# Kernel optimization log

Hardware: AMD Instinct MI355X
Metric: run time of the kernel (lower is better)

Reference implementation:

```python
import jax, jax.numpy as jnp
import numpy as np

D_IN = 1024
D_OUT = 1024
NUM_HEADS = 16
D_HEAD = D_OUT // NUM_HEADS


def setup_inputs() -> dict:
    key = jax.random.key(0)
    ks = jax.random.split(key, 6)
    s = 0.02
    return {
        "x": jax.random.normal(ks[0], (2, 2048, D_IN), dtype=jnp.float32),
        "W_q": jax.random.normal(ks[1], (D_IN, D_OUT), dtype=jnp.float32) * s,
        "W_k": jax.random.normal(ks[2], (D_IN, D_OUT), dtype=jnp.float32) * s,
        "W_v": jax.random.normal(ks[3], (D_IN, D_OUT), dtype=jnp.float32) * s,
        "W_o": jax.random.normal(ks[4], (D_OUT, D_OUT), dtype=jnp.float32) * s,
        "b_o": jax.random.normal(ks[5], (D_OUT,), dtype=jnp.float32) * s,
    }


def reference(x, W_q, W_k, W_v, W_o, b_o):
    B, T, _ = x.shape
    # qkv projections (no bias), split heads -> [B, H, T, d_head]
    def split_heads(t):
        return t.reshape(B, T, NUM_HEADS, D_HEAD).transpose(0, 2, 1, 3)
    q = split_heads(x @ W_q)
    k = split_heads(x @ W_k)
    v = split_heads(x @ W_v)
    # full causal scores [B, H, T, T]
    scores = jnp.einsum("bhqd,bhkd->bhqk", q, k)
    causal = jnp.triu(jnp.ones((T, T), dtype=bool), k=1)
    scores = jnp.where(causal, -jnp.inf, scores)
    attn = jax.nn.softmax(scores / np.sqrt(D_HEAD).astype(np.float32), axis=-1)
    # dropout rate is 0.0 -> identity
    ctx = jnp.einsum("bhqk,bhkd->bhqd", attn, v)
    ctx = ctx.transpose(0, 2, 1, 3).reshape(B, T, D_OUT)
    return ctx @ W_o + b_o
```

## Files before the change

kernel.cpp:

```cpp
#include <hip/hip_runtime.h>
#include <hip/hip_bf16.h>
#include <cstdint>

#define SEQ_T 2048
#define DMODEL 1024
#define NHEAD 16
#define DHEAD 64

typedef __attribute__((ext_vector_type(8))) __bf16 bf16x8;
typedef __attribute__((ext_vector_type(4))) float floatx4;

static __device__ __forceinline__ uint16_t f2bf(float f) {
    union { float f; uint32_t u; } v; v.f = f;
    uint32_t r = v.u + 0x7FFFu + ((v.u >> 16) & 1u);
    return (uint16_t)(r >> 16);
}

__global__ void mha_cvt(const float* __restrict__ x, uint16_t* __restrict__ xb,
                        const float* __restrict__ W0, const float* __restrict__ W1,
                        const float* __restrict__ W2, const float* __restrict__ W3,
                        uint16_t* __restrict__ T0, uint16_t* __restrict__ T1,
                        uint16_t* __restrict__ T2, uint16_t* __restrict__ T3) {
    if (blockIdx.z == 4) {
        int base = (blockIdx.y * 16 + blockIdx.x) * 256 + threadIdx.x;
#pragma unroll
        for (int i = 0; i < 16; ++i) {
            int idx = base + i * 65536;
            float4 f = ((const float4*)x)[idx];
            union { uint16_t u[4]; uint64_t v; } o;
            o.u[0] = f2bf(f.x); o.u[1] = f2bf(f.y); o.u[2] = f2bf(f.z); o.u[3] = f2bf(f.w);
            ((uint64_t*)xb)[idx] = o.v;
        }
        return;
    }
    const float* W; uint16_t* Tt; float sc;
    switch (blockIdx.z) {
        case 0: W = W0; Tt = T0; sc = 0.125f * 1.44269504089f; break;
        case 1: W = W1; Tt = T1; sc = 1.f; break;
        case 2: W = W2; Tt = T2; sc = 1.f; break;
        default: W = W3; Tt = T3; sc = 1.f; break;
    }
    __shared__ float tile[64][65];
    const int c  = threadIdx.x & 63;
    const int r0 = threadIdx.x >> 6;
    const int R0 = blockIdx.y * 64, C0 = blockIdx.x * 64;
#pragma unroll
    for (int rr = 0; rr < 16; ++rr) {
        int r = r0 + rr * 4;
        tile[r][c] = W[(size_t)(R0 + r) * DMODEL + C0 + c];
    }
    __syncthreads();
#pragma unroll
    for (int rr = 0; rr < 16; ++rr) {
        int r = r0 + rr * 4;
        Tt[(size_t)(C0 + r) * DMODEL + R0 + c] = f2bf(tile[c][r] * sc);
    }
}

template<int MODE>
__device__ __forceinline__ void gemm_bk64_body(
    const uint16_t* __restrict__ A, const uint16_t* __restrict__ Bt,
    uint16_t* __restrict__ outB) {
    const int K = DMODEL, N = DMODEL;
    extern __shared__ char smem[];
    uint16_t* As = (uint16_t*)smem;
    uint16_t* Bs = (uint16_t*)(smem + 8192);
    const int tid  = threadIdx.x;
    const int wave = tid >> 6;
    const int lane = tid & 63;
    const int m0 = blockIdx.y * 64;
    const int n0 = blockIdx.x * 128;
    const int lr   = lane & 15;
    const int quad = lane >> 4;

    floatx4 acc[4][2];
#pragma unroll
    for (int i = 0; i < 4; ++i)
#pragma unroll
        for (int j = 0; j < 2; ++j) acc[i][j] = (floatx4)0.0f;

    for (int k0 = 0; k0 < K; k0 += 64) {
#pragma unroll
        for (int i = 0; i < 2; ++i) {
            int c = i * 256 + tid;
            int r = c >> 3, s = (c & 7) ^ (r & 7);
            const uint16_t* g = A + (size_t)(m0 + r) * K + k0 + s * 8;
            __builtin_amdgcn_global_load_lds((const __attribute__((address_space(1))) void*)g,
                                             (__attribute__((address_space(3))) void*)(As + (size_t)c * 8), 16, 0, 0);
        }
#pragma unroll
        for (int i = 0; i < 4; ++i) {
            int c = i * 256 + tid;
            int r = c >> 3, s = (c & 7) ^ (r & 7);
            const uint16_t* g = Bt + (size_t)(n0 + r) * K + k0 + s * 8;
            __builtin_amdgcn_global_load_lds((const __attribute__((address_space(1))) void*)g,
                                             (__attribute__((address_space(3))) void*)(Bs + (size_t)c * 8), 16, 0, 0);
        }
        __syncthreads();
#pragma unroll
        for (int ks = 0; ks < 2; ++ks) {
            bf16x8 af[4], bfr[2];
#pragma unroll
            for (int mi = 0; mi < 4; ++mi) {
                int row = mi * 16 + lr;
                af[mi] = *(const bf16x8*)&As[row * 64 + (((ks * 4 + quad) ^ (row & 7)) << 3)];
            }
#pragma unroll
            for (int ni = 0; ni < 2; ++ni) {
                int row = wave * 32 + ni * 16 + lr;
                bfr[ni] = *(const bf16x8*)&Bs[row * 64 + (((ks * 4 + quad) ^ (row & 7)) << 3)];
            }
#pragma unroll
            for (int mi = 0; mi < 4; ++mi)
#pragma unroll
                for (int ni = 0; ni < 2; ++ni)
                    acc[mi][ni] = __builtin_amdgcn_mfma_f32_16x16x32_bf16(af[mi], bfr[ni], acc[mi][ni], 0, 0, 0);
        }
        __syncthreads();
    }
    if constexpr (MODE == 1) {
        uint16_t* Ct = (uint16_t*)smem;
        const int bb = m0 >> 11, t0 = m0 & 2047;
#pragma unroll
        for (int mi = 0; mi < 4; ++mi)
#pragma unroll
            for (int ni = 0; ni < 2; ++ni) {
                int cl = wave * 32 + ni * 16 + lr;
                int tl = mi * 16 + quad * 4;
                int tls = tl ^ ((cl & 3) << 4);
                union { uint16_t u[4]; uint64_t v8; } pk;
#pragma unroll
                for (int r = 0; r < 4; ++r) pk.u[r] = f2bf(acc[mi][ni][r]);
                *(uint64_t*)&Ct[cl * 72 + tls] = pk.v8;
            }
        __syncthreads();
#pragma unroll
        for (int k = 0; k < 4; ++k) {
            int c = k * 256 + tid;
            int cl = c >> 3, off = (c & 7) * 8;
            int offs = off ^ ((cl & 3) << 4);
            uint4 v = *(const uint4*)&Ct[cl * 72 + offs];
            *(uint4*)&outB[((size_t)(bb * 1024 + n0 + cl)) * 2048 + t0 + off] = v;
        }
    } else {
#pragma unroll
        for (int mi = 0; mi < 4; ++mi)
#pragma unroll
            for (int ni = 0; ni < 2; ++ni) {
                int col = n0 + wave * 32 + ni * 16 + lr;
#pragma unroll
                for (int r = 0; r < 4; ++r) {
                    int row = m0 + mi * 16 + quad * 4 + r;
                    outB[(size_t)row * N + col] = f2bf(acc[mi][ni][r]);
                }
            }
    }
}

__global__ __launch_bounds__(256) void mha_gemm_qkv(
    const uint16_t* __restrict__ A,
    const uint16_t* __restrict__ Wq, const uint16_t* __restrict__ Wk, const uint16_t* __restrict__ Wv,
    uint16_t* __restrict__ Q, uint16_t* __restrict__ K, uint16_t* __restrict__ Vt) {
    switch (blockIdx.z) {
        case 0:  gemm_bk64_body<0>(A, Wq, Q);  break;
        case 1:  gemm_bk64_body<0>(A, Wk, K);  break;
        default: gemm_bk64_body<1>(A, Wv, Vt); break;
    }
}

__global__ __launch_bounds__(512) void mha_gemm_out(
    const uint16_t* __restrict__ A, const uint16_t* __restrict__ Wot,
    float* __restrict__ out, const float* __restrict__ bias) {
    const int K = DMODEL, N = DMODEL;
    extern __shared__ char smem[];
    uint16_t* As = (uint16_t*)smem;
    uint16_t* Bs = (uint16_t*)(smem + 8192);
    const int tid  = threadIdx.x;
    const int wave = tid >> 6;
    const int lane = tid & 63;
    const int m0 = blockIdx.y * 64;
    const int n0 = blockIdx.x * 128;
    const int lr   = lane & 15;
    const int quad = lane >> 4;
    const int wm = wave >> 2, wn = wave & 3;

    floatx4 acc[2][2];
#pragma unroll
    for (int i = 0; i < 2; ++i)
#pragma unroll
        for (int j = 0; j < 2; ++j) acc[i][j] = (floatx4)0.0f;

    for (int k0 = 0; k0 < K; k0 += 64) {
        {
            int c = tid;
            int r = c >> 3, s = (c & 7) ^ (r & 7);
            const uint16_t* g = A + (size_t)(m0 + r) * K + k0 + s * 8;
            __builtin_amdgcn_global_load_lds((const __attribute__((address_space(1))) void*)g,
                                             (__attribute__((address_space(3))) void*)(As + (size_t)c * 8), 16, 0, 0);
        }
#pragma unroll
        for (int i = 0; i < 2; ++i) {
            int c = i * 512 + tid;
            int r = c >> 3, s = (c & 7) ^ (r & 7);
            const uint16_t* g = Wot + (size_t)(n0 + r) * K + k0 + s * 8;
            __builtin_amdgcn_global_load_lds((const __attribute__((address_space(1))) void*)g,
                                             (__attribute__((address_space(3))) void*)(Bs + (size_t)c * 8), 16, 0, 0);
        }
        __syncthreads();
#pragma unroll
        for (int ks = 0; ks < 2; ++ks) {
            bf16x8 af[2], bfr[2];
#pragma unroll
            for (int mi = 0; mi < 2; ++mi) {
                int row = wm * 32 + mi * 16 + lr;
                af[mi] = *(const bf16x8*)&As[row * 64 + (((ks * 4 + quad) ^ (row & 7)) << 3)];
            }
#pragma unroll
            for (int ni = 0; ni < 2; ++ni) {
                int row = wn * 32 + ni * 16 + lr;
                bfr[ni] = *(const bf16x8*)&Bs[row * 64 + (((ks * 4 + quad) ^ (row & 7)) << 3)];
            }
#pragma unroll
            for (int mi = 0; mi < 2; ++mi)
#pragma unroll
                for (int ni = 0; ni < 2; ++ni)
                    acc[mi][ni] = __builtin_amdgcn_mfma_f32_16x16x32_bf16(af[mi], bfr[ni], acc[mi][ni], 0, 0, 0);
        }
        __syncthreads();
    }
#pragma unroll
    for (int mi = 0; mi < 2; ++mi)
#pragma unroll
        for (int ni = 0; ni < 2; ++ni) {
            int col = n0 + wn * 32 + ni * 16 + lr;
            float bv = bias[col];
#pragma unroll
            for (int r = 0; r < 4; ++r) {
                int row = m0 + wm * 32 + mi * 16 + quad * 4 + r;
                out[(size_t)row * N + col] = acc[mi][ni][r] + bv;
            }
        }
}

__global__ __launch_bounds__(256) void mha_attn_mfma(
    const uint16_t* __restrict__ Q, const uint16_t* __restrict__ K,
    const uint16_t* __restrict__ Vt, uint16_t* __restrict__ ctx) {
    __shared__ alignas(16) uint16_t Ks[3][64 * 64];
    __shared__ alignas(16) uint16_t Vs[3][64 * 64];
    __shared__ alignas(16) uint16_t Pb[64 * 64];

    const int tid  = threadIdx.x;
    const int wave = tid >> 6;
    const int lane = tid & 63;
    const int lr   = lane & 15;
    const int quad = lane >> 4;
    const int h  = blockIdx.x;
    const int p  = blockIdx.y;
    const int b  = blockIdx.z;
    const int jH = 31 - p, jL = p;
    const int TH = jH + 1;
    const int TL = jL + 1;
    const int Ttot = TH + TL;

    const uint16_t* kbase[2];
    const uint16_t* vbase[2];
#pragma unroll
    for (int i = 0; i < 2; ++i) {
        int c = i * 256 + tid;
        int row = c >> 3, cs = c & 7;
        int csk = cs ^ (row & 7);
        kbase[i] = K  + ((size_t)(b * SEQ_T) + row) * DMODEL + h * DHEAD + csk * 8;
        vbase[i] = Vt + ((size_t)(b * 1024 + h * DHEAD + row)) * 2048 + csk * 8;
    }

    int wrow = jH * 64 + wave * 16;
    bf16x8 qf0, qf1;
    {
        const size_t qb = ((size_t)(b * SEQ_T) + wrow + lr) * DMODEL + h * DHEAD;
        qf0 = *(const bf16x8*)(Q + qb + quad * 8);
        qf1 = *(const bf16x8*)(Q + qb + 32 + quad * 8);
    }
    bf16x8 ones;
#pragma unroll
    for (int i = 0; i < 8; ++i) ones[i] = (__bf16)1.0f;

    floatx4 o[4];
#pragma unroll
    for (int nt = 0; nt < 4; ++nt) o[nt] = (floatx4)0.0f;
    floatx4 lacc = (floatx4)0.0f;

    auto kvof = [&](int t) { return ((t < TH) ? t : (t - TH)) * 64; };
    auto stage = [&](int kv0, int buf) {
#pragma unroll
        for (int i = 0; i < 2; ++i) {
            const uint16_t* gk = kbase[i] + (size_t)kv0 * DMODEL;
            const uint16_t* gv = vbase[i] + kv0;
            uint16_t* lk = &Ks[buf][(i * 256 + wave * 64) * 8];
            uint16_t* lv = &Vs[buf][(i * 256 + wave * 64) * 8];
            __builtin_amdgcn_global_load_lds((const __attribute__((address_space(1))) void*)gk,
                                             (__attribute__((address_space(3))) void*)lk, 16, 0, 0);
            __builtin_amdgcn_global_load_lds((const __attribute__((address_space(1))) void*)gv,
                                             (__attribute__((address_space(3))) void*)lv, 16, 0, 0);
        }
    };
    auto epilogue = [&]() {
        float linv[4];
#pragma unroll
        for (int r = 0; r < 4; ++r) linv[r] = 1.f / lacc[r];
#pragma unroll
        for (int nt = 0; nt < 4; ++nt)
#pragma unroll
            for (int r = 0; r < 4; ++r) {
                size_t addr = ((size_t)(b * SEQ_T) + wrow + quad * 4 + r) * DMODEL + h * DHEAD + nt * 16 + lr;
                ctx[addr] = f2bf(o[nt][r] * linv[r]);
            }
    };

    stage(kvof(0), 0);
    stage(kvof(1), 1);
    __builtin_amdgcn_s_waitcnt(0x0F74);
    __builtin_amdgcn_s_barrier();

    for (int t = 0; t < Ttot; ++t) {
        if (t + 2 < Ttot) stage(kvof(t + 2), (t + 2) % 3);
        const int cur = t % 3;
        const int kv0 = kvof(t);

        floatx4 s[4];
#pragma unroll
        for (int nt = 0; nt < 4; ++nt) {
            s[nt] = (floatx4)0.0f;
            int krow = nt * 16 + lr;
#pragma unroll
            for (int ks = 0; ks < 2; ++ks) {
                bf16x8 kf = *(const bf16x8*)&Ks[cur][krow * 64 + (((ks * 4 + quad) ^ (lr & 7)) * 8)];
                s[nt] = __builtin_amdgcn_mfma_f32_16x16x32_bf16(ks ? qf1 : qf0, kf, s[nt], 0, 0, 0);
            }
        }
        if (kv0 + 63 > wrow) {
#pragma unroll
            for (int nt = 0; nt < 4; ++nt) {
                int kcol = kv0 + nt * 16 + lr;
#pragma unroll
                for (int r = 0; r < 4; ++r) {
                    int qrow = wrow + quad * 4 + r;
                    if (kcol > qrow) s[nt][r] = -3e38f;
                }
            }
        }
#pragma unroll
        for (int nt = 0; nt < 4; ++nt)
#pragma unroll
            for (int r = 0; r < 4; ++r) {
                float pe = __builtin_amdgcn_exp2f(s[nt][r]);
                int row = wave * 16 + quad * 4 + r;
                int cc  = (nt * 2 + (lr >> 3)) ^ (row & 7);
                Pb[row * 64 + cc * 8 + (lr & 7)] = (uint16_t)(__float_as_uint(pe) >> 16);
            }
#pragma unroll
        for (int ks = 0; ks < 2; ++ks) {
            int prow = wave * 16 + lr;
            bf16x8 pfr = *(const bf16x8*)&Pb[prow * 64 + (((ks * 4 + quad) ^ (prow & 7)) * 8)];
            lacc = __builtin_amdgcn_mfma_f32_16x16x32_bf16(pfr, ones, lacc, 0, 0, 0);
#pragma unroll
            for (int nt = 0; nt < 4; ++nt) {
                int vrow = nt * 16 + lr;
                bf16x8 vf = *(const bf16x8*)&Vs[cur][vrow * 64 + (((ks * 4 + quad) ^ (lr & 7)) * 8)];
                o[nt] = __builtin_amdgcn_mfma_f32_16x16x32_bf16(pfr, vf, o[nt], 0, 0, 0);
            }
        }
        if (t == TH - 1) {
            epilogue();
            wrow = jL * 64 + wave * 16;
            const size_t qb = ((size_t)(b * SEQ_T) + wrow + lr) * DMODEL + h * DHEAD;
            qf0 = *(const bf16x8*)(Q + qb + quad * 8);
            qf1 = *(const bf16x8*)(Q + qb + 32 + quad * 8);
#pragma unroll
            for (int nt = 0; nt < 4; ++nt) o[nt] = (floatx4)0.0f;
            lacc = (floatx4)0.0f;
        }
        if (t + 2 < Ttot) {
            __builtin_amdgcn_s_waitcnt(0x0F74);
            __builtin_amdgcn_s_barrier();
        } else if (t + 1 < Ttot) {
            __builtin_amdgcn_s_waitcnt(0x0F70);
            __builtin_amdgcn_s_barrier();
        }
    }
    epilogue();
}

extern "C" void kernel_launch(void* const* d_in, const int* in_sizes, int n_in,
                              void* d_out, int out_size, void* d_ws, size_t ws_size,
                              hipStream_t stream) {
    const float* x  = (const float*)d_in[0];
    const float* Wq = (const float*)d_in[1];
    const float* Wk = (const float*)d_in[2];
    const float* Wv = (const float*)d_in[3];
    const float* Wo = (const float*)d_in[4];
    const float* bo = (const float*)d_in[5];
    float* out = (float*)d_out;

    char* ws = (char*)d_ws;
    const size_t SZ_X = (size_t)4096 * DMODEL * 2;
    const size_t SZ_W = (size_t)DMODEL * DMODEL * 2;
    size_t off = 0;
    uint16_t* xb  = (uint16_t*)(ws + off); off += SZ_X;
    uint16_t* wqt = (uint16_t*)(ws + off); off += SZ_W;
    uint16_t* wkt = (uint16_t*)(ws + off); off += SZ_W;
    uint16_t* wvt = (uint16_t*)(ws + off); off += SZ_W;
    uint16_t* wot = (uint16_t*)(ws + off); off += SZ_W;
    uint16_t* Qb  = (uint16_t*)(ws + off); off += SZ_X;
    uint16_t* Kb  = (uint16_t*)(ws + off); off += SZ_X;
    uint16_t* Vtb = (uint16_t*)(ws + off); off += SZ_X;
    uint16_t* Cb  = (uint16_t*)(ws + off); off += SZ_X;
    (void)ws_size; (void)in_sizes; (void)n_in; (void)out_size;

    mha_cvt<<<dim3(16, 16, 5), 256, 0, stream>>>(x, xb, Wq, Wk, Wv, Wo, wqt, wkt, wvt, wot);
    mha_gemm_qkv<<<dim3(8, 64, 3), 256, 24576, stream>>>(xb, wqt, wkt, wvt, Qb, Kb, Vtb);
    mha_attn_mfma<<<dim3(NHEAD, 16, 2), 256, 0, stream>>>(Qb, Kb, Vtb, Cb);
    mha_gemm_out<<<dim3(8, 64), 512, 24576, stream>>>(Cb, wot, out, bo);
}
```

Measured before the change: 177.5 us.

## Split attention KV tiles across two wave groups with 128-wide tiles and LDS combine

The attention kernel moves to 512 threads. Two groups of four waves each handle half of a 128-key tile, so each block needs fewer sequential iterations (17 instead of up to 33) and keeps double buffering in place of triple buffering. Partial outputs and row sums from the second group are combined through LDS before the store. In exchange there are extra barriers and LDS traffic at the combine, larger LDS tiles that may lower occupancy, and masking now covers whole 128 tiles, which can waste work on the diagonal.

```diff
diff --git a/kernel.cpp b/kernel.cpp
--- a/kernel.cpp
+++ b/kernel.cpp
@@ -242,38 +242,38 @@
         }
 }
 
-__global__ __launch_bounds__(256) void mha_attn_mfma(
+__global__ __launch_bounds__(512, 4) void mha_attn_mfma(
     const uint16_t* __restrict__ Q, const uint16_t* __restrict__ K,
     const uint16_t* __restrict__ Vt, uint16_t* __restrict__ ctx) {
-    __shared__ alignas(16) uint16_t Ks[3][64 * 64];
-    __shared__ alignas(16) uint16_t Vs[3][64 * 64];
-    __shared__ alignas(16) uint16_t Pb[64 * 64];
+    __shared__ alignas(16) uint16_t KsB[2][128 * 64];
+    __shared__ alignas(16) uint16_t VsB[2][64 * 128];
+    __shared__ alignas(16) uint16_t Pb[64 * 128];
 
     const int tid  = threadIdx.x;
     const int wave = tid >> 6;
     const int lane = tid & 63;
     const int lr   = lane & 15;
     const int quad = lane >> 4;
+    const int qw   = wave & 3;
+    const int kvh  = wave >> 2;
     const int h  = blockIdx.x;
     const int p  = blockIdx.y;
     const int b  = blockIdx.z;
     const int jH = 31 - p, jL = p;
-    const int TH = jH + 1;
-    const int TL = jL + 1;
-    const int Ttot = TH + TL;
-
-    const uint16_t* kbase[2];
-    const uint16_t* vbase[2];
+    const int TH = (33 - p) >> 1;
+
+    const uint16_t* kg[2];
+    const uint16_t* vg[2];
 #pragma unroll
     for (int i = 0; i < 2; ++i) {
-        int c = i * 256 + tid;
-        int row = c >> 3, cs = c & 7;
-        int csk = cs ^ (row & 7);
-        kbase[i] = K  + ((size_t)(b * SEQ_T) + row) * DMODEL + h * DHEAD + csk * 8;
-        vbase[i] = Vt + ((size_t)(b * 1024 + h * DHEAD + row)) * 2048 + csk * 8;
-    }
-
-    int wrow = jH * 64 + wave * 16;
+        int c  = i * 512 + tid;
+        int rk = c >> 3, sk = (c & 7) ^ (rk & 7);
+        kg[i] = K + ((size_t)(b * SEQ_T) + rk) * DMODEL + h * DHEAD + sk * 8;
+        int rv = c >> 4, hv = (c >> 3) & 1, sv = (c & 7) ^ (rv & 7);
+        vg[i] = Vt + ((size_t)(b * 1024 + h * DHEAD + rv)) * 2048 + hv * 64 + sv * 8;
+    }
+
+    int wrow = jH * 64 + qw * 16;
     bf16x8 qf0, qf1;
     {
         const size_t qb = ((size_t)(b * SEQ_T) + wrow + lr) * DMODEL + h * DHEAD;
@@ -289,58 +289,78 @@
     for (int nt = 0; nt < 4; ++nt) o[nt] = (floatx4)0.0f;
     floatx4 lacc = (floatx4)0.0f;
 
-    auto kvof = [&](int t) { return ((t < TH) ? t : (t - TH)) * 64; };
     auto stage = [&](int kv0, int buf) {
 #pragma unroll
         for (int i = 0; i < 2; ++i) {
-            const uint16_t* gk = kbase[i] + (size_t)kv0 * DMODEL;
-            const uint16_t* gv = vbase[i] + kv0;
-            uint16_t* lk = &Ks[buf][(i * 256 + wave * 64) * 8];
-            uint16_t* lv = &Vs[buf][(i * 256 + wave * 64) * 8];
-            __builtin_amdgcn_global_load_lds((const __attribute__((address_space(1))) void*)gk,
-                                             (__attribute__((address_space(3))) void*)lk, 16, 0, 0);
-            __builtin_amdgcn_global_load_lds((const __attribute__((address_space(1))) void*)gv,
-                                             (__attribute__((address_space(3))) void*)lv, 16, 0, 0);
+            int c = i * 512 + tid;
+            __builtin_amdgcn_global_load_lds(
+                (const __attribute__((address_space(1))) void*)(kg[i] + (size_t)kv0 * DMODEL),
+                (__attribute__((address_space(3))) void*)(&KsB[buf][c * 8]), 16, 0, 0);
+            __builtin_amdgcn_global_load_lds(
+                (const __attribute__((address_space(1))) void*)(vg[i] + kv0),
+                (__attribute__((address_space(3))) void*)(&VsB[buf][c * 8]), 16, 0, 0);
         }
     };
-    auto epilogue = [&]() {
-        float linv[4];
-#pragma unroll
-        for (int r = 0; r < 4; ++r) linv[r] = 1.f / lacc[r];
-#pragma unroll
-        for (int nt = 0; nt < 4; ++nt)
-#pragma unroll
-            for (int r = 0; r < 4; ++r) {
-                size_t addr = ((size_t)(b * SEQ_T) + wrow + quad * 4 + r) * DMODEL + h * DHEAD + nt * 16 + lr;
-                ctx[addr] = f2bf(o[nt][r] * linv[r]);
-            }
+
+    auto combine_store = [&](int cur) {
+        __syncthreads();
+        float* Pbf = (float*)Pb;
+        float* Lf  = (float*)&VsB[cur][0];
+        if (kvh == 1) {
+#pragma unroll
+            for (int nt = 0; nt < 4; ++nt)
+#pragma unroll
+                for (int r = 0; r < 4; ++r)
+                    Pbf[(qw * 16 + quad * 4 + r) * 64 + ((nt ^ quad) * 16 + lr)] = o[nt][r];
+            if (lr == 0) {
+#pragma unroll
+                for (int r = 0; r < 4; ++r) Lf[qw * 16 + quad * 4 + r] = lacc[r];
+            }
+        }
+        __syncthreads();
+        if (kvh == 0) {
+            float linv[4];
+#pragma unroll
+            for (int r = 0; r < 4; ++r)
+                linv[r] = 1.f / (lacc[r] + Lf[qw * 16 + quad * 4 + r]);
+#pragma unroll
+            for (int nt = 0; nt < 4; ++nt)
+#pragma unroll
+                for (int r = 0; r < 4; ++r) {
+                    float ov = o[nt][r] + Pbf[(qw * 16 + quad * 4 + r) * 64 + ((nt ^ quad) * 16 + lr)];
+                    size_t addr = ((size_t)(b * SEQ_T) + wrow + quad * 4 + r) * DMODEL + h * DHEAD + nt * 16 + lr;
+                    ctx[addr] = f2bf(ov * linv[r]);
+                }
+        }
     };
 
-    stage(kvof(0), 0);
-    stage(kvof(1), 1);
-    __builtin_amdgcn_s_waitcnt(0x0F74);
-    __builtin_amdgcn_s_barrier();
-
-    for (int t = 0; t < Ttot; ++t) {
-        if (t + 2 < Ttot) stage(kvof(t + 2), (t + 2) % 3);
-        const int cur = t % 3;
-        const int kv0 = kvof(t);
-
+    stage(0, 0);
+    __syncthreads();
+
+    for (int t = 0; t < 17; ++t) {
+        const int cur = t & 1;
+        const int kv0 = (t < TH ? t : t - TH) * 128;
+        if (t + 1 < 17) {
+            const int tn = t + 1;
+            stage((tn < TH ? tn : tn - TH) * 128, tn & 1);
+        }
+
+        const int kvb = kv0 + kvh * 64;
         floatx4 s[4];
 #pragma unroll
         for (int nt = 0; nt < 4; ++nt) {
             s[nt] = (floatx4)0.0f;
-            int krow = nt * 16 + lr;
+            int krow = kvh * 64 + nt * 16 + lr;
 #pragma unroll
             for (int ks = 0; ks < 2; ++ks) {
-                bf16x8 kf = *(const bf16x8*)&Ks[cur][krow * 64 + (((ks * 4 + quad) ^ (lr & 7)) * 8)];
+                bf16x8 kf = *(const bf16x8*)&KsB[cur][krow * 64 + (((ks * 4 + quad) ^ (lr & 7)) * 8)];
                 s[nt] = __builtin_amdgcn_mfma_f32_16x16x32_bf16(ks ? qf1 : qf0, kf, s[nt], 0, 0, 0);
             }
         }
-        if (kv0 + 63 > wrow) {
+        if (kvb + 63 > wrow) {
 #pragma unroll
             for (int nt = 0; nt < 4; ++nt) {
-                int kcol = kv0 + nt * 16 + lr;
+                int kcol = kvb + nt * 16 + lr;
 #pragma unroll
                 for (int r = 0; r < 4; ++r) {
                     int qrow = wrow + quad * 4 + r;
@@ -353,25 +373,25 @@
 #pragma unroll
             for (int r = 0; r < 4; ++r) {
                 float pe = __builtin_amdgcn_exp2f(s[nt][r]);
-                int row = wave * 16 + quad * 4 + r;
-                int cc  = (nt * 2 + (lr >> 3)) ^ (row & 7);
-                Pb[row * 64 + cc * 8 + (lr & 7)] = (uint16_t)(__float_as_uint(pe) >> 16);
+                int row = qw * 16 + quad * 4 + r;
+                int cc  = kvh * 8 + ((nt * 2 + (lr >> 3)) ^ (row & 7));
+                Pb[row * 128 + cc * 8 + (lr & 7)] = (uint16_t)(__float_as_uint(pe) >> 16);
             }
 #pragma unroll
         for (int ks = 0; ks < 2; ++ks) {
-            int prow = wave * 16 + lr;
-            bf16x8 pfr = *(const bf16x8*)&Pb[prow * 64 + (((ks * 4 + quad) ^ (prow & 7)) * 8)];
+            int prow = qw * 16 + lr;
+            bf16x8 pfr = *(const bf16x8*)&Pb[prow * 128 + ((kvh * 8 + ((ks * 4 + quad) ^ (prow & 7))) * 8)];
             lacc = __builtin_amdgcn_mfma_f32_16x16x32_bf16(pfr, ones, lacc, 0, 0, 0);
 #pragma unroll
             for (int nt = 0; nt < 4; ++nt) {
                 int vrow = nt * 16 + lr;
-                bf16x8 vf = *(const bf16x8*)&Vs[cur][vrow * 64 + (((ks * 4 + quad) ^ (lr & 7)) * 8)];
+                bf16x8 vf = *(const bf16x8*)&VsB[cur][vrow * 128 + ((kvh * 8 + ((ks * 4 + quad) ^ (lr & 7))) * 8)];
                 o[nt] = __builtin_amdgcn_mfma_f32_16x16x32_bf16(pfr, vf, o[nt], 0, 0, 0);
             }
         }
         if (t == TH - 1) {
-            epilogue();
-            wrow = jL * 64 + wave * 16;
+            combine_store(cur);
+            wrow = jL * 64 + qw * 16;
             const size_t qb = ((size_t)(b * SEQ_T) + wrow + lr) * DMODEL + h * DHEAD;
             qf0 = *(const bf16x8*)(Q + qb + quad * 8);
             qf1 = *(const bf16x8*)(Q + qb + 32 + quad * 8);
@@ -379,15 +399,9 @@
             for (int nt = 0; nt < 4; ++nt) o[nt] = (floatx4)0.0f;
             lacc = (floatx4)0.0f;
         }
-        if (t + 2 < Ttot) {
-            __builtin_amdgcn_s_waitcnt(0x0F74);
-            __builtin_amdgcn_s_barrier();
-        } else if (t + 1 < Ttot) {
-            __builtin_amdgcn_s_waitcnt(0x0F70);
-            __builtin_amdgcn_s_barrier();
-        }
-    }
-    epilogue();
+        if (t + 1 < 17) __syncthreads();
+    }
+    combine_store(0);
 }
 
 extern "C" void kernel_launch(void* const* d_in, const int* in_sizes, int n_in,
@@ -418,6 +432,6 @@
 
     mha_cvt<<<dim3(16, 16, 5), 256, 0, stream>>>(x, xb, Wq, Wk, Wv, Wo, wqt, wkt, wvt, wot);
     mha_gemm_qkv<<<dim3(8, 64, 3), 256, 24576, stream>>>(xb, wqt, wkt, wvt, Qb, Kb, Vtb);
-    mha_attn_mfma<<<dim3(NHEAD, 16, 2), 256, 0, stream>>>(Qb, Kb, Vtb, Cb);
+    mha_attn_mfma<<<dim3(NHEAD, 16, 2), 512, 0, stream>>>(Qb, Kb, Vtb, Cb);
     mha_gemm_out<<<dim3(8, 64), 512, 24576, stream>>>(Cb, wot, out, bo);
 }
```

Result: faster. 171.1 us (-3.6%).
